# Kernel optimization log

Measured on AMD Instinct MI355X. Metric: run time of the kernel, lower is better.

Reference implementation:

```python
import jax, jax.numpy as jnp
import numpy as np

EPS = 1e-5

def conv1x1(x, w, b):
    # x: (B,C,H,W), w: (O,C), b: (O,)
    return jnp.einsum('bchw,oc->bohw', x, w) + b[None, :, None, None]

def instance_norm(x):
    mu = jnp.mean(x, axis=(2, 3), keepdims=True)
    var = jnp.var(x, axis=(2, 3), keepdims=True)
    return (x - mu) / jnp.sqrt(var + EPS)

def setup_inputs() -> dict:
    key = jax.random.key(0)
    C = 256
    ks = jax.random.split(key, 16)
    def w(k):
        return jax.random.normal(k, (C, C), dtype=jnp.float32) * 0.02
    def b(k):
        return jax.random.normal(k, (C,), dtype=jnp.float32) * 0.01
    return {
        'x': jax.random.normal(ks[0], (8, C, 128, 128), dtype=jnp.float32),
        'wq1': w(ks[1]), 'bq1': b(ks[2]), 'wq2': w(ks[3]), 'bq2': b(ks[4]),
        'wk1': w(ks[5]), 'bk1': b(ks[6]), 'wk2': w(ks[7]), 'bk2': b(ks[8]),
        'wv': w(ks[9]), 'bv': b(ks[10]),
        'wg': w(ks[11]), 'bg': b(ks[12]),
        'wo': w(ks[13]), 'bo': b(ks[14]),
    }

def reference(x, wq1, bq1, wq2, bq2, wk1, bk1, wk2, bk2, wv, bv, wg, bg, wo, bo):
    head = 4
    B, C, H, W = x.shape
    c = C // head  # per-head channels
    n = H * W
    x = instance_norm(x)
    q = jax.nn.softplus(conv1x1(jax.nn.gelu(conv1x1(x, wq1, bq1), approximate=False), wq2, bq2))
    k = jax.nn.softplus(conv1x1(jax.nn.gelu(conv1x1(x, wk1, bk1), approximate=False), wk2, bk2))
    v = jax.nn.gelu(conv1x1(x, wv, bv), approximate=False)
    g = jax.nn.gelu(conv1x1(x, wg, bg), approximate=False)
    # b (head c) h w -> b head c (h w)
    q = q.reshape(B, head, c, n)
    kk = k.reshape(B, head, c, n)
    vv = v.reshape(B, head, c, n)
    kv = jnp.einsum('bhcn,bhdn->bhcd', kk, vv)  # (B,head,c,c)
    scale = 1.0 / jnp.sqrt(jnp.float32(c))
    z = jnp.einsum('bhcn,bhc->bhn', q, kk.sum(axis=-1)) * scale
    z = 1.0 / (z + jnp.float32(n))
    out = jnp.einsum('bhcn,bhcd->bhdn', q, kv) * scale
    out = (out + vv) * z[:, :, None, :]
    out = out.reshape(B, C, H, W)
    out = out * g
    return conv1x1(out, wo, bo)
```

## Files before the change

### kernel.cpp

```cpp
#include <hip/hip_runtime.h>
#include <stdint.h>

typedef short bf8 __attribute__((ext_vector_type(8)));
typedef short s4v __attribute__((ext_vector_type(4)));
typedef float f32x4 __attribute__((ext_vector_type(4)));

__device__ __forceinline__ short f2bf(float f){
  union { float f; unsigned u; } c; c.f = f;
  unsigned r = (c.u + 0x7fffu + ((c.u >> 16) & 1u)) >> 16;
  return (short)r;
}
__device__ __forceinline__ float bf2f(short s){
  union { unsigned u; float f; } c; c.u = ((unsigned)(unsigned short)s) << 16;
  return c.f;
}
__device__ __forceinline__ void gload16(const void* g, void* l){
  __builtin_amdgcn_global_load_lds((const __attribute__((address_space(1))) uint32_t*)g,
                                   (__attribute__((address_space(3))) uint32_t*)l, 16, 0, 0);
}
__device__ __forceinline__ float fast_erf(float x){
  const float s = fabsf(x);
  const float t = __builtin_amdgcn_rcpf(fmaf(0.3275911f, s, 1.0f));
  float p = fmaf(1.061405429f, t, -1.453152027f);
  p = fmaf(p, t, 1.421413741f);
  p = fmaf(p, t, -0.284496736f);
  p = fmaf(p, t, 0.254829592f);
  p = p * t;
  const float e = __expf(-s * s);
  return copysignf(fmaf(-p, e, 1.0f), x);
}
__device__ __forceinline__ float act_gelu(float x){
  return 0.5f * x * (1.0f + fast_erf(x * 0.70710678118654752f));
}
__device__ __forceinline__ float act_softplus(float x){
  const float e = __expf(-fabsf(x));
  return fmaxf(x, 0.0f) + __logf(1.0f + e);
}

__global__ __launch_bounds__(256) void k_stats(const float* __restrict__ x,
                                               float* __restrict__ mu, float* __restrict__ rsig){
  const int row = blockIdx.x;
  const float4* xr = (const float4*)(x + (size_t)row * 16384);
  float s1 = 0.f, s2 = 0.f;
  for (int i = threadIdx.x; i < 4096; i += 256){
    float4 v = xr[i];
    s1 += v.x + v.y + v.z + v.w;
    s2 += v.x*v.x + v.y*v.y + v.z*v.z + v.w*v.w;
  }
  __shared__ float a1[256], a2[256];
  a1[threadIdx.x] = s1; a2[threadIdx.x] = s2; __syncthreads();
  for (int s = 128; s > 0; s >>= 1){
    if (threadIdx.x < s){ a1[threadIdx.x] += a1[threadIdx.x+s]; a2[threadIdx.x] += a2[threadIdx.x+s]; }
    __syncthreads();
  }
  if (threadIdx.x == 0){
    float m = a1[0] * (1.0f/16384.0f);
    float v = a2[0] * (1.0f/16384.0f) - m*m;
    mu[row] = m; rsig[row] = rsqrtf(v + 1e-5f);
  }
}

__global__ __launch_bounds__(256) void k_normt(const float* __restrict__ x, const float* __restrict__ mu,
                                               const float* __restrict__ rsig, short* __restrict__ xn){
  const int n0 = blockIdx.x * 64, c0 = blockIdx.y * 64, b = blockIdx.z;
  __shared__ short lt[64][68];
  const int t = threadIdx.x;
  const int nj = (t & 15) * 4, cb = t >> 4;
#pragma unroll
  for (int it = 0; it < 4; ++it){
    const int ci = cb + it * 16;
    const int row = b * 256 + c0 + ci;
    const float m = mu[row], rs = rsig[row];
    float4 v = *(const float4*)(x + (size_t)row * 16384 + n0 + nj);
    s4v o;
    o[0] = f2bf((v.x - m) * rs); o[1] = f2bf((v.y - m) * rs);
    o[2] = f2bf((v.z - m) * rs); o[3] = f2bf((v.w - m) * rs);
    *(s4v*)(&lt[ci][nj]) = o;
  }
  __syncthreads();
#pragma unroll
  for (int p = 0; p < 2; ++p){
    const int q = p * 256 + t;
    const int nl = q >> 3, c8 = (q & 7) * 8;
    bf8 o;
#pragma unroll
    for (int j = 0; j < 8; ++j) o[j] = lt[c8 + j][nl];
    *(bf8*)(xn + ((size_t)(b * 16384 + n0 + nl)) * 256 + c0 + c8) = o;
  }
}

__global__ __launch_bounds__(256) void k_wconv(const float* w0, const float* w1, const float* w2,
                                               const float* w3, const float* w4, const float* w5,
                                               const float* w6, short* __restrict__ wb){
  const int gid = blockIdx.x * 256 + threadIdx.x;
  const int mat = gid >> 14, r4 = gid & 16383;
  const float* srcs[7] = {w0, w1, w2, w3, w4, w5, w6};
  float4 v = *(const float4*)(srcs[mat] + (size_t)r4 * 4);
  s4v o; o[0] = f2bf(v.x); o[1] = f2bf(v.y); o[2] = f2bf(v.z); o[3] = f2bf(v.w);
  *(s4v*)(wb + (size_t)mat * 65536 + r4 * 4) = o;
}

template<int ACT, int OUTMODE>
__global__ __launch_bounds__(256, 2)
void k_gemm(const short* __restrict__ A, const short* __restrict__ W,
            const float* __restrict__ bias, void* __restrict__ outv){
  __shared__ short sm[12288];
  short* sA = sm;
  short* sB = sm + 4096;
  const int t = threadIdx.x, l = t & 63, w = t >> 6;
  const int wr = w >> 1, wc = w & 1;
  const int lm = l & 15, lk = l >> 4;
  const size_t m0 = (size_t)blockIdx.x * 128;
  const int swz = ((lk ^ ((lm >> 1) & 3)) << 4);
  f32x4 acc[4][8] = {};

  for (int ks = 0; ks < 8; ++ks){
    const int k0 = ks * 32;
#pragma unroll
    for (int p = 0; p < 2; ++p){
      const int q = p * 256 + t, r = q >> 2, kc = q & 3;
      gload16(A + (m0 + r) * 256 + k0 + ((kc ^ ((r >> 1) & 3)) << 3),
              (char*)sA + (p * 256 + w * 64) * 16);
    }
#pragma unroll
    for (int p = 0; p < 4; ++p){
      const int q = p * 256 + t, r = q >> 2, kc = q & 3;
      gload16(W + (size_t)r * 256 + k0 + ((kc ^ ((r >> 1) & 3)) << 3),
              (char*)sB + (p * 256 + w * 64) * 16);
    }
    __syncthreads();
    bf8 af[4], bfv[8];
#pragma unroll
    for (int mi = 0; mi < 4; ++mi)
      af[mi] = *(const bf8*)((const char*)sA + (wr * 64 + mi * 16 + lm) * 64 + swz);
#pragma unroll
    for (int ni = 0; ni < 8; ++ni)
      bfv[ni] = *(const bf8*)((const char*)sB + (wc * 128 + ni * 16 + lm) * 64 + swz);
#pragma unroll
    for (int mi = 0; mi < 4; ++mi)
#pragma unroll
      for (int ni = 0; ni < 8; ++ni){
        if constexpr (OUTMODE == 0)
          acc[mi][ni] = __builtin_amdgcn_mfma_f32_16x16x32_bf16(bfv[ni], af[mi], acc[mi][ni], 0, 0, 0);
        else
          acc[mi][ni] = __builtin_amdgcn_mfma_f32_16x16x32_bf16(af[mi], bfv[ni], acc[mi][ni], 0, 0, 0);
      }
    __syncthreads();
  }

  if constexpr (OUTMODE == 0){
    short* outp = (short*)outv;
#pragma unroll
    for (int ni = 0; ni < 8; ++ni){
      const int ob = wc * 128 + ni * 16 + lk * 4;
      const float4 b4 = *(const float4*)(bias + ob);
#pragma unroll
      for (int mi = 0; mi < 4; ++mi){
        const int px = wr * 64 + mi * 16 + lm;
        s4v o4;
#pragma unroll
        for (int j = 0; j < 4; ++j){
          float v = acc[mi][ni][j] + ((const float*)&b4)[j];
          if (ACT == 1) v = act_gelu(v);
          else if (ACT == 2) v = act_softplus(v);
          o4[j] = f2bf(v);
        }
        *(s4v*)(outp + (m0 + px) * 256 + ob) = o4;
      }
    }
  } else {
    float* outp = (float*)outv;
    const size_t b = m0 >> 14;
    const int nb = (int)(m0 & 16383);
#pragma unroll
    for (int mi = 0; mi < 4; ++mi){
      const int np = nb + wr * 64 + mi * 16 + lk * 4;
#pragma unroll
      for (int ni = 0; ni < 8; ++ni){
        const int o = wc * 128 + ni * 16 + lm;
        const float bi = bias[o];
        float4 v;
        v.x = acc[mi][ni][0] + bi; v.y = acc[mi][ni][1] + bi;
        v.z = acc[mi][ni][2] + bi; v.w = acc[mi][ni][3] + bi;
        *(float4*)(outp + ((b * 256 + o) * 16384 + np)) = v;
      }
    }
  }
}

__global__ __launch_bounds__(256, 2)
void k_chain(const short* __restrict__ A, const short* __restrict__ W1, const float* __restrict__ b1,
             const short* __restrict__ W2, const float* __restrict__ b2, short* __restrict__ out){
  __shared__ short sA[64 * 32];
  __shared__ short sB[256 * 32];
  __shared__ short h1[64 * 256];
  const int t = threadIdx.x, l = t & 63, w = t >> 6;
  const int lm = l & 15, lk = l >> 4;
  const size_t m0 = (size_t)blockIdx.x * 64;
  const int swz = ((lk ^ ((lm >> 1) & 3)) << 4);
  f32x4 acc[4][4] = {};

  for (int ks = 0; ks < 8; ++ks){
    const int k0 = ks * 32;
    {
      const int r = t >> 2, kc = t & 3;
      gload16(A + (m0 + r) * 256 + k0 + ((kc ^ ((r >> 1) & 3)) << 3),
              (char*)sA + w * 1024);
    }
#pragma unroll
    for (int p = 0; p < 4; ++p){
      const int q = p * 256 + t, r = q >> 2, kc = q & 3;
      gload16(W1 + (size_t)r * 256 + k0 + ((kc ^ ((r >> 1) & 3)) << 3),
              (char*)sB + (p * 256 + w * 64) * 16);
    }
    __syncthreads();
    bf8 af[4], bfv[4];
#pragma unroll
    for (int mi = 0; mi < 4; ++mi)
      af[mi] = *(const bf8*)((const char*)sA + (mi * 16 + lm) * 64 + swz);
#pragma unroll
    for (int ni = 0; ni < 4; ++ni)
      bfv[ni] = *(const bf8*)((const char*)sB + (w * 64 + ni * 16 + lm) * 64 + swz);
#pragma unroll
    for (int mi = 0; mi < 4; ++mi)
#pragma unroll
      for (int ni = 0; ni < 4; ++ni)
        acc[mi][ni] = __builtin_amdgcn_mfma_f32_16x16x32_bf16(bfv[ni], af[mi], acc[mi][ni], 0, 0, 0);
    __syncthreads();
  }
#pragma unroll
  for (int ni = 0; ni < 4; ++ni){
    const int ob = w * 64 + ni * 16 + lk * 4;
    const float4 b4 = *(const float4*)(b1 + ob);
#pragma unroll
    for (int mi = 0; mi < 4; ++mi){
      const int px = mi * 16 + lm;
      s4v o4;
#pragma unroll
      for (int j = 0; j < 4; ++j)
        o4[j] = f2bf(act_gelu(acc[mi][ni][j] + ((const float*)&b4)[j]));
      const int slot = (ob >> 3) ^ (px & 7);
      *(s4v*)((char*)h1 + px * 512 + (slot << 4) + (ob & 4) * 2) = o4;
      acc[mi][ni] = (f32x4){0.f, 0.f, 0.f, 0.f};
    }
  }
  __syncthreads();

  for (int ks = 0; ks < 8; ++ks){
    const int k0 = ks * 32;
#pragma unroll
    for (int p = 0; p < 4; ++p){
      const int q = p * 256 + t, r = q >> 2, kc = q & 3;
      gload16(W2 + (size_t)r * 256 + k0 + ((kc ^ ((r >> 1) & 3)) << 3),
              (char*)sB + (p * 256 + w * 64) * 16);
    }
    __syncthreads();
    bf8 af[4], bfv[4];
#pragma unroll
    for (int mi = 0; mi < 4; ++mi){
      const int row = mi * 16 + lm;
      const int slot = (ks * 4 + lk) ^ (row & 7);
      af[mi] = *(const bf8*)((const char*)h1 + row * 512 + (slot << 4));
    }
#pragma unroll
    for (int ni = 0; ni < 4; ++ni)
      bfv[ni] = *(const bf8*)((const char*)sB + (w * 64 + ni * 16 + lm) * 64 + swz);
#pragma unroll
    for (int mi = 0; mi < 4; ++mi)
#pragma unroll
      for (int ni = 0; ni < 4; ++ni)
        acc[mi][ni] = __builtin_amdgcn_mfma_f32_16x16x32_bf16(bfv[ni], af[mi], acc[mi][ni], 0, 0, 0);
    __syncthreads();
  }
#pragma unroll
  for (int ni = 0; ni < 4; ++ni){
    const int ob = w * 64 + ni * 16 + lk * 4;
    const float4 b4 = *(const float4*)(b2 + ob);
#pragma unroll
    for (int mi = 0; mi < 4; ++mi){
      const int px = mi * 16 + lm;
      s4v o4;
#pragma unroll
      for (int j = 0; j < 4; ++j)
        o4[j] = f2bf(act_softplus(acc[mi][ni][j] + ((const float*)&b4)[j]));
      *(s4v*)(out + (m0 + px) * 256 + ob) = o4;
    }
  }
}

__global__ __launch_bounds__(256) void k_kv(const short* __restrict__ kg, const short* __restrict__ vg,
                                            float* __restrict__ kvpart, float* __restrict__ kspart){
  const int s = blockIdx.x, h = blockIdx.y, b = blockIdx.z;
  __shared__ short sk[64 * 72], sv[64 * 72];
  __shared__ float pl[256][8];
  const int t = threadIdx.x, l = t & 63, w = t >> 6;
  const int lm = l & 15, lk = l >> 4;
  float ksp[8];
#pragma unroll
  for (int j = 0; j < 8; ++j) ksp[j] = 0.f;
  f32x4 acc[4] = {};
  const size_t rowbase = ((size_t)b * 16384 + s * 2048) * 256 + h * 64;

  for (int tt = 0; tt < 32; ++tt){
    __syncthreads();
#pragma unroll
    for (int p = 0; p < 2; ++p){
      const int q = p * 256 + t;
      const int nl = q >> 3, c8 = (q & 7) * 8;
      bf8 kvv = *(const bf8*)(kg + rowbase + (size_t)(tt * 64 + nl) * 256 + c8);
      bf8 vvv = *(const bf8*)(vg + rowbase + (size_t)(tt * 64 + nl) * 256 + c8);
#pragma unroll
      for (int j = 0; j < 8; ++j){
        sk[(c8 + j) * 72 + nl] = kvv[j];
        sv[(c8 + j) * 72 + nl] = vvv[j];
        ksp[j] += bf2f(kvv[j]);
      }
    }
    __syncthreads();
#pragma unroll
    for (int ks = 0; ks < 2; ++ks){
      bf8 ak = *(const bf8*)((const char*)sk + (w * 16 + lm) * 144 + ks * 64 + lk * 16);
#pragma unroll
      for (int ni = 0; ni < 4; ++ni){
        bf8 bv = *(const bf8*)((const char*)sv + (ni * 16 + lm) * 144 + ks * 64 + lk * 16);
        acc[ni] = __builtin_amdgcn_mfma_f32_16x16x32_bf16(ak, bv, acc[ni], 0, 0, 0);
      }
    }
  }
#pragma unroll
  for (int j = 0; j < 8; ++j) pl[t][j] = ksp[j];
  __syncthreads();
  const size_t slot = (size_t)(b * 4 + h) * 8 + s;
  if (t < 64){
    float sum = 0.f;
    const int g8 = t >> 3, j = t & 7;
    for (int m = 0; m < 32; ++m) sum += pl[m * 8 + g8][j];
    kspart[slot * 64 + t] = sum;
  }
  float* kvp = kvpart + slot * 4096;
#pragma unroll
  for (int ni = 0; ni < 4; ++ni)
#pragma unroll
    for (int j = 0; j < 4; ++j){
      const int c = w * 16 + lk * 4 + j, d = ni * 16 + lm;
      kvp[c * 64 + d] = acc[ni][j];
    }
}

__global__ __launch_bounds__(256) void k_kvred(const float* __restrict__ kvpart, const float* __restrict__ kspart,
                                               short* __restrict__ kvT, float* __restrict__ ksum_s){
  const int gid = blockIdx.x * 256 + threadIdx.x;
#pragma unroll
  for (int i = 0; i < 8; ++i){
    const int o = gid * 8 + i;
    const int bh = o >> 12, rem = o & 4095, d = rem >> 6, c = rem & 63;
    float sum = 0.f;
#pragma unroll
    for (int s = 0; s < 8; ++s) sum += kvpart[((size_t)bh * 8 + s) * 4096 + c * 64 + d];
    kvT[o] = f2bf(sum * 0.125f);
  }
  if (gid < 2048){
    float sum = 0.f;
#pragma unroll
    for (int s = 0; s < 8; ++s) sum += kspart[((size_t)(gid >> 6) * 8 + s) * 64 + (gid & 63)];
    ksum_s[gid] = sum * 0.125f;
  }
}

__global__ __launch_bounds__(256, 3) void k_attn(const short* __restrict__ qg, const short* __restrict__ vg,
                                                 const short* __restrict__ gg, const short* __restrict__ kvT,
                                                 const float* __restrict__ ksum_s, short* __restrict__ y){
  const int n0 = blockIdx.x * 64, b = blockIdx.y;
  __shared__ short skv[256 * 72];
  __shared__ float sz[256];
  __shared__ float sks[256];
  const int t = threadIdx.x, l = t & 63, w = t >> 6;
  const int lm = l & 15, lk = l >> 4;
  const size_t mrow = (size_t)b * 16384 + n0;
  const int h = w;

  const short* kvb = kvT + (size_t)b * 16384;
#pragma unroll
  for (int it = 0; it < 8; ++it){
    const int q = it * 256 + t, r = q >> 3, c8 = (q & 7) * 8;
    *(bf8*)((char*)skv + r * 144 + c8 * 2) = *(const bf8*)(kvb + r * 64 + c8);
  }
  sks[t] = ksum_s[b * 256 + t];
  __syncthreads();

  {
    const int p = l;
    float dot = 0.f;
#pragma unroll
    for (int cc = 0; cc < 8; ++cc){
      bf8 qv = *(const bf8*)(qg + (mrow + p) * 256 + h * 64 + cc * 8);
#pragma unroll
      for (int j = 0; j < 8; ++j) dot += bf2f(qv[j]) * sks[h * 64 + cc * 8 + j];
    }
    sz[h * 64 + p] = 1.0f / (dot + 16384.0f);
  }

  f32x4 acc[4][4] = {};
#pragma unroll
  for (int ks = 0; ks < 2; ++ks){
    bf8 aq[4];
#pragma unroll
    for (int mi = 0; mi < 4; ++mi)
      aq[mi] = *(const bf8*)(qg + (mrow + mi * 16 + lm) * 256 + h * 64 + ks * 32 + lk * 8);
#pragma unroll
    for (int ni = 0; ni < 4; ++ni){
      bf8 bk = *(const bf8*)((const char*)skv + (h * 64 + ni * 16 + lm) * 144 + ks * 64 + lk * 16);
#pragma unroll
      for (int mi = 0; mi < 4; ++mi)
        acc[mi][ni] = __builtin_amdgcn_mfma_f32_16x16x32_bf16(bk, aq[mi], acc[mi][ni], 0, 0, 0);
    }
  }
#pragma unroll
  for (int mi = 0; mi < 4; ++mi){
    const int px = mi * 16 + lm;
    const float zf = sz[h * 64 + px];
    const size_t base = (mrow + px) * 256;
#pragma unroll
    for (int ni = 0; ni < 4; ++ni){
      const int ch = h * 64 + ni * 16 + lk * 4;
      s4v v4 = *(const s4v*)(vg + base + ch);
      s4v g4 = *(const s4v*)(gg + base + ch);
      s4v o4;
#pragma unroll
      for (int j = 0; j < 4; ++j)
        o4[j] = f2bf((acc[mi][ni][j] + bf2f(v4[j])) * zf * bf2f(g4[j]));
      *(s4v*)(y + base + ch) = o4;
    }
  }
}

extern "C" void kernel_launch(void* const* d_in, const int* in_sizes, int n_in,
                              void* d_out, int out_size, void* d_ws, size_t ws_size,
                              hipStream_t stream){
  (void)in_sizes; (void)n_in; (void)out_size; (void)ws_size;
  const float* x   = (const float*)d_in[0];
  const float* wq1 = (const float*)d_in[1];
  const float* bq1 = (const float*)d_in[2];
  const float* wq2 = (const float*)d_in[3];
  const float* bq2 = (const float*)d_in[4];
  const float* wk1 = (const float*)d_in[5];
  const float* bk1 = (const float*)d_in[6];
  const float* wk2 = (const float*)d_in[7];
  const float* bk2 = (const float*)d_in[8];
  const float* wv  = (const float*)d_in[9];
  const float* bv  = (const float*)d_in[10];
  const float* wg  = (const float*)d_in[11];
  const float* bg  = (const float*)d_in[12];
  const float* wo  = (const float*)d_in[13];
  const float* bo  = (const float*)d_in[14];

  char* ws = (char*)d_ws;
  float* mu     = (float*)(ws + 0);
  float* rsig   = (float*)(ws + 8192);
  short* wb     = (short*)(ws + 16384);
  float* kvpart = (float*)(ws + 933888);
  float* kspart = (float*)(ws + 5128192);
  short* kvT    = (short*)(ws + 5193728);
  float* ksum_s = (float*)(ws + 5455872);
  short* B0 = (short*)(ws + 8388608);
  short* B1 = B0 + 33554432;
  short* B2 = B1 + 33554432;
  short* B3 = B2 + 33554432;

  k_wconv<<<448, 256, 0, stream>>>(wq1, wq2, wk1, wk2, wv, wg, wo, wb);
  k_stats<<<2048, 256, 0, stream>>>(x, mu, rsig);
  k_normt<<<dim3(256, 4, 8), 256, 0, stream>>>(x, mu, rsig, B0);
  k_chain<<<2048, 256, 0, stream>>>(B0, wb + 0 * 65536, bq1, wb + 1 * 65536, bq2, B2);
  k_chain<<<2048, 256, 0, stream>>>(B0, wb + 2 * 65536, bk1, wb + 3 * 65536, bk2, B3);
  k_gemm<1, 0><<<1024, 256, 0, stream>>>(B0, wb + 4 * 65536, bv, B1);
  k_kv<<<dim3(8, 4, 8), 256, 0, stream>>>(B3, B1, kvpart, kspart);
  k_kvred<<<64, 256, 0, stream>>>(kvpart, kspart, kvT, ksum_s);
  k_gemm<1, 0><<<1024, 256, 0, stream>>>(B0, wb + 5 * 65536, bg, B3);
  k_attn<<<dim3(256, 8), 256, 0, stream>>>(B2, B1, B3, kvT, ksum_s, B0);
  k_gemm<0, 1><<<1024, 256, 0, stream>>>(B0, wb + 6 * 65536, bo, d_out);
}
```

Measured before the change: 494.4 us.

## Fuse stats into transpose pass and load GEMM operands directly from global

Instance-norm statistics are now computed as per-block partial sums inside the transpose pass. The raw bf16 transpose is then normalized in place by a separate elementwise kernel after a small reduction kernel, so the fp32 input is read only once instead of twice. The GEMM, chain and attention kernels drop LDS staging and barriers and load MFMA operands straight from global memory, relying on cache reuse. k_attn occupancy is also raised. The risks are extra bf16 rounding before normalization, an added read-write pass over the activation buffer, and uncoalesced, uncached-reuse global loads in the GEMMs.

```diff
diff --git a/kernel.cpp b/kernel.cpp
--- a/kernel.cpp
+++ b/kernel.cpp
@@ -13,10 +13,6 @@
 __device__ __forceinline__ float bf2f(short s){
   union { unsigned u; float f; } c; c.u = ((unsigned)(unsigned short)s) << 16;
   return c.f;
-}
-__device__ __forceinline__ void gload16(const void* g, void* l){
-  __builtin_amdgcn_global_load_lds((const __attribute__((address_space(1))) uint32_t*)g,
-                                   (__attribute__((address_space(3))) uint32_t*)l, 16, 0, 0);
 }
 __device__ __forceinline__ float fast_erf(float x){
   const float s = fabsf(x);
@@ -37,45 +33,22 @@
   return fmaxf(x, 0.0f) + __logf(1.0f + e);
 }
 
-__global__ __launch_bounds__(256) void k_stats(const float* __restrict__ x,
-                                               float* __restrict__ mu, float* __restrict__ rsig){
-  const int row = blockIdx.x;
-  const float4* xr = (const float4*)(x + (size_t)row * 16384);
-  float s1 = 0.f, s2 = 0.f;
-  for (int i = threadIdx.x; i < 4096; i += 256){
-    float4 v = xr[i];
-    s1 += v.x + v.y + v.z + v.w;
-    s2 += v.x*v.x + v.y*v.y + v.z*v.z + v.w*v.w;
-  }
-  __shared__ float a1[256], a2[256];
-  a1[threadIdx.x] = s1; a2[threadIdx.x] = s2; __syncthreads();
-  for (int s = 128; s > 0; s >>= 1){
-    if (threadIdx.x < s){ a1[threadIdx.x] += a1[threadIdx.x+s]; a2[threadIdx.x] += a2[threadIdx.x+s]; }
-    __syncthreads();
-  }
-  if (threadIdx.x == 0){
-    float m = a1[0] * (1.0f/16384.0f);
-    float v = a2[0] * (1.0f/16384.0f) - m*m;
-    mu[row] = m; rsig[row] = rsqrtf(v + 1e-5f);
-  }
-}
-
-__global__ __launch_bounds__(256) void k_normt(const float* __restrict__ x, const float* __restrict__ mu,
-                                               const float* __restrict__ rsig, short* __restrict__ xn){
+__global__ __launch_bounds__(256) void k_statst(const float* __restrict__ x, short* __restrict__ xt,
+                                                float* __restrict__ ps1, float* __restrict__ ps2){
   const int n0 = blockIdx.x * 64, c0 = blockIdx.y * 64, b = blockIdx.z;
   __shared__ short lt[64][68];
-  const int t = threadIdx.x;
-  const int nj = (t & 15) * 4, cb = t >> 4;
+  const int t = threadIdx.x, nj = (t & 15) * 4, cb = t >> 4;
+  float s1[4] = {0.f,0.f,0.f,0.f}, s2[4] = {0.f,0.f,0.f,0.f};
 #pragma unroll
   for (int it = 0; it < 4; ++it){
     const int ci = cb + it * 16;
     const int row = b * 256 + c0 + ci;
-    const float m = mu[row], rs = rsig[row];
     float4 v = *(const float4*)(x + (size_t)row * 16384 + n0 + nj);
     s4v o;
-    o[0] = f2bf((v.x - m) * rs); o[1] = f2bf((v.y - m) * rs);
-    o[2] = f2bf((v.z - m) * rs); o[3] = f2bf((v.w - m) * rs);
+    o[0] = f2bf(v.x); o[1] = f2bf(v.y); o[2] = f2bf(v.z); o[3] = f2bf(v.w);
     *(s4v*)(&lt[ci][nj]) = o;
+    s1[it] += v.x + v.y + v.z + v.w;
+    s2[it] += v.x*v.x + v.y*v.y + v.z*v.z + v.w*v.w;
   }
   __syncthreads();
 #pragma unroll
@@ -85,7 +58,64 @@
     bf8 o;
 #pragma unroll
     for (int j = 0; j < 8; ++j) o[j] = lt[c8 + j][nl];
-    *(bf8*)(xn + ((size_t)(b * 16384 + n0 + nl)) * 256 + c0 + c8) = o;
+    *(bf8*)(xt + ((size_t)(b * 16384 + n0 + nl)) * 256 + c0 + c8) = o;
+  }
+#pragma unroll
+  for (int it = 0; it < 4; ++it){
+#pragma unroll
+    for (int off = 8; off > 0; off >>= 1){
+      s1[it] += __shfl_down(s1[it], off);
+      s2[it] += __shfl_down(s2[it], off);
+    }
+  }
+  if ((t & 15) == 0){
+#pragma unroll
+    for (int it = 0; it < 4; ++it){
+      const int c = c0 + cb + it * 16;
+      ps1[((size_t)(b * 256 + c)) * 256 + blockIdx.x] = s1[it];
+      ps2[((size_t)(b * 256 + c)) * 256 + blockIdx.x] = s2[it];
+    }
+  }
+}
+
+__global__ __launch_bounds__(256) void k_red(const float* __restrict__ ps1, const float* __restrict__ ps2,
+                                             float* __restrict__ mu, float* __restrict__ rsig){
+  const int bc = blockIdx.x;
+  const int t = threadIdx.x;
+  __shared__ float a1[256], a2[256];
+  a1[t] = ps1[(size_t)bc * 256 + t];
+  a2[t] = ps2[(size_t)bc * 256 + t];
+  __syncthreads();
+  for (int s = 128; s > 0; s >>= 1){
+    if (t < s){ a1[t] += a1[t+s]; a2[t] += a2[t+s]; }
+    __syncthreads();
+  }
+  if (t == 0){
+    float m = a1[0] * (1.0f/16384.0f);
+    float v = a2[0] * (1.0f/16384.0f) - m*m;
+    mu[bc] = m; rsig[bc] = rsqrtf(v + 1e-5f);
+  }
+}
+
+__global__ __launch_bounds__(256) void k_norm(short* xn, const float* __restrict__ mu,
+                                              const float* __restrict__ rsig){
+  const int g = blockIdx.x * 256 + threadIdx.x;
+#pragma unroll
+  for (int pass = 0; pass < 8; ++pass){
+    const int idx = g + pass * 524288;
+    const int bn = idx >> 5, c8 = idx & 31;
+    const int b = bn >> 14;
+    const float* mp = mu + b * 256 + c8 * 8;
+    const float* rp = rsig + b * 256 + c8 * 8;
+    float4 m0 = *(const float4*)mp, m1 = *(const float4*)(mp + 4);
+    float4 r0 = *(const float4*)rp, r1 = *(const float4*)(rp + 4);
+    float mm[8] = {m0.x,m0.y,m0.z,m0.w,m1.x,m1.y,m1.z,m1.w};
+    float rr[8] = {r0.x,r0.y,r0.z,r0.w,r1.x,r1.y,r1.z,r1.w};
+    bf8 v = *(const bf8*)(xn + (size_t)idx * 8);
+    bf8 o;
+#pragma unroll
+    for (int j = 0; j < 8; ++j) o[j] = f2bf((bf2f(v[j]) - mm[j]) * rr[j]);
+    *(bf8*)(xn + (size_t)idx * 8) = o;
   }
 }
 
@@ -104,38 +134,23 @@
 __global__ __launch_bounds__(256, 2)
 void k_gemm(const short* __restrict__ A, const short* __restrict__ W,
             const float* __restrict__ bias, void* __restrict__ outv){
-  __shared__ short sm[12288];
-  short* sA = sm;
-  short* sB = sm + 4096;
   const int t = threadIdx.x, l = t & 63, w = t >> 6;
   const int wr = w >> 1, wc = w & 1;
   const int lm = l & 15, lk = l >> 4;
   const size_t m0 = (size_t)blockIdx.x * 128;
-  const int swz = ((lk ^ ((lm >> 1) & 3)) << 4);
+  const short* Ab = A + (m0 + wr * 64 + lm) * 256 + lk * 8;
+  const short* Wb = W + (size_t)(wc * 128 + lm) * 256 + lk * 8;
   f32x4 acc[4][8] = {};
 
+#pragma unroll 2
   for (int ks = 0; ks < 8; ++ks){
-    const int k0 = ks * 32;
-#pragma unroll
-    for (int p = 0; p < 2; ++p){
-      const int q = p * 256 + t, r = q >> 2, kc = q & 3;
-      gload16(A + (m0 + r) * 256 + k0 + ((kc ^ ((r >> 1) & 3)) << 3),
-              (char*)sA + (p * 256 + w * 64) * 16);
-    }
-#pragma unroll
-    for (int p = 0; p < 4; ++p){
-      const int q = p * 256 + t, r = q >> 2, kc = q & 3;
-      gload16(W + (size_t)r * 256 + k0 + ((kc ^ ((r >> 1) & 3)) << 3),
-              (char*)sB + (p * 256 + w * 64) * 16);
-    }
-    __syncthreads();
     bf8 af[4], bfv[8];
 #pragma unroll
     for (int mi = 0; mi < 4; ++mi)
-      af[mi] = *(const bf8*)((const char*)sA + (wr * 64 + mi * 16 + lm) * 64 + swz);
+      af[mi] = *(const bf8*)(Ab + mi * 16 * 256 + ks * 32);
 #pragma unroll
     for (int ni = 0; ni < 8; ++ni)
-      bfv[ni] = *(const bf8*)((const char*)sB + (wc * 128 + ni * 16 + lm) * 64 + swz);
+      bfv[ni] = *(const bf8*)(Wb + ni * 16 * 256 + ks * 32);
 #pragma unroll
     for (int mi = 0; mi < 4; ++mi)
 #pragma unroll
@@ -145,7 +160,6 @@
         else
           acc[mi][ni] = __builtin_amdgcn_mfma_f32_16x16x32_bf16(af[mi], bfv[ni], acc[mi][ni], 0, 0, 0);
       }
-    __syncthreads();
   }
 
   if constexpr (OUTMODE == 0){
@@ -191,42 +205,29 @@
 __global__ __launch_bounds__(256, 2)
 void k_chain(const short* __restrict__ A, const short* __restrict__ W1, const float* __restrict__ b1,
              const short* __restrict__ W2, const float* __restrict__ b2, short* __restrict__ out){
-  __shared__ short sA[64 * 32];
-  __shared__ short sB[256 * 32];
   __shared__ short h1[64 * 256];
   const int t = threadIdx.x, l = t & 63, w = t >> 6;
   const int lm = l & 15, lk = l >> 4;
   const size_t m0 = (size_t)blockIdx.x * 64;
-  const int swz = ((lk ^ ((lm >> 1) & 3)) << 4);
+  const short* Ab = A + (m0 + lm) * 256 + lk * 8;
+  const short* W1b = W1 + (size_t)(w * 64 + lm) * 256 + lk * 8;
+  const short* W2b = W2 + (size_t)(w * 64 + lm) * 256 + lk * 8;
   f32x4 acc[4][4] = {};
 
+#pragma unroll 2
   for (int ks = 0; ks < 8; ++ks){
-    const int k0 = ks * 32;
-    {
-      const int r = t >> 2, kc = t & 3;
-      gload16(A + (m0 + r) * 256 + k0 + ((kc ^ ((r >> 1) & 3)) << 3),
-              (char*)sA + w * 1024);
-    }
-#pragma unroll
-    for (int p = 0; p < 4; ++p){
-      const int q = p * 256 + t, r = q >> 2, kc = q & 3;
-      gload16(W1 + (size_t)r * 256 + k0 + ((kc ^ ((r >> 1) & 3)) << 3),
-              (char*)sB + (p * 256 + w * 64) * 16);
-    }
-    __syncthreads();
     bf8 af[4], bfv[4];
 #pragma unroll
     for (int mi = 0; mi < 4; ++mi)
-      af[mi] = *(const bf8*)((const char*)sA + (mi * 16 + lm) * 64 + swz);
+      af[mi] = *(const bf8*)(Ab + mi * 16 * 256 + ks * 32);
 #pragma unroll
     for (int ni = 0; ni < 4; ++ni)
-      bfv[ni] = *(const bf8*)((const char*)sB + (w * 64 + ni * 16 + lm) * 64 + swz);
+      bfv[ni] = *(const bf8*)(W1b + ni * 16 * 256 + ks * 32);
 #pragma unroll
     for (int mi = 0; mi < 4; ++mi)
 #pragma unroll
       for (int ni = 0; ni < 4; ++ni)
         acc[mi][ni] = __builtin_amdgcn_mfma_f32_16x16x32_bf16(bfv[ni], af[mi], acc[mi][ni], 0, 0, 0);
-    __syncthreads();
   }
 #pragma unroll
   for (int ni = 0; ni < 4; ++ni){
@@ -246,15 +247,8 @@
   }
   __syncthreads();
 
+#pragma unroll 2
   for (int ks = 0; ks < 8; ++ks){
-    const int k0 = ks * 32;
-#pragma unroll
-    for (int p = 0; p < 4; ++p){
-      const int q = p * 256 + t, r = q >> 2, kc = q & 3;
-      gload16(W2 + (size_t)r * 256 + k0 + ((kc ^ ((r >> 1) & 3)) << 3),
-              (char*)sB + (p * 256 + w * 64) * 16);
-    }
-    __syncthreads();
     bf8 af[4], bfv[4];
 #pragma unroll
     for (int mi = 0; mi < 4; ++mi){
@@ -264,13 +258,12 @@
     }
 #pragma unroll
     for (int ni = 0; ni < 4; ++ni)
-      bfv[ni] = *(const bf8*)((const char*)sB + (w * 64 + ni * 16 + lm) * 64 + swz);
+      bfv[ni] = *(const bf8*)(W2b + ni * 16 * 256 + ks * 32);
 #pragma unroll
     for (int mi = 0; mi < 4; ++mi)
 #pragma unroll
       for (int ni = 0; ni < 4; ++ni)
         acc[mi][ni] = __builtin_amdgcn_mfma_f32_16x16x32_bf16(bfv[ni], af[mi], acc[mi][ni], 0, 0, 0);
-    __syncthreads();
   }
 #pragma unroll
   for (int ni = 0; ni < 4; ++ni){
@@ -367,11 +360,10 @@
   }
 }
 
-__global__ __launch_bounds__(256, 3) void k_attn(const short* __restrict__ qg, const short* __restrict__ vg,
+__global__ __launch_bounds__(256, 4) void k_attn(const short* __restrict__ qg, const short* __restrict__ vg,
                                                  const short* __restrict__ gg, const short* __restrict__ kvT,
                                                  const float* __restrict__ ksum_s, short* __restrict__ y){
   const int n0 = blockIdx.x * 64, b = blockIdx.y;
-  __shared__ short skv[256 * 72];
   __shared__ float sz[256];
   __shared__ float sks[256];
   const int t = threadIdx.x, l = t & 63, w = t >> 6;
@@ -379,14 +371,7 @@
   const size_t mrow = (size_t)b * 16384 + n0;
   const int h = w;
 
-  const short* kvb = kvT + (size_t)b * 16384;
-#pragma unroll
-  for (int it = 0; it < 8; ++it){
-    const int q = it * 256 + t, r = q >> 3, c8 = (q & 7) * 8;
-    *(bf8*)((char*)skv + r * 144 + c8 * 2) = *(const bf8*)(kvb + r * 64 + c8);
-  }
   sks[t] = ksum_s[b * 256 + t];
-  __syncthreads();
 
   {
     const int p = l;
@@ -400,6 +385,7 @@
     sz[h * 64 + p] = 1.0f / (dot + 16384.0f);
   }
 
+  const short* kvb = kvT + (size_t)b * 16384;
   f32x4 acc[4][4] = {};
 #pragma unroll
   for (int ks = 0; ks < 2; ++ks){
@@ -409,7 +395,7 @@
       aq[mi] = *(const bf8*)(qg + (mrow + mi * 16 + lm) * 256 + h * 64 + ks * 32 + lk * 8);
 #pragma unroll
     for (int ni = 0; ni < 4; ++ni){
-      bf8 bk = *(const bf8*)((const char*)skv + (h * 64 + ni * 16 + lm) * 144 + ks * 64 + lk * 16);
+      bf8 bk = *(const bf8*)(kvb + (size_t)(h * 64 + ni * 16 + lm) * 64 + ks * 32 + lk * 8);
 #pragma unroll
       for (int mi = 0; mi < 4; ++mi)
         acc[mi][ni] = __builtin_amdgcn_mfma_f32_16x16x32_bf16(bk, aq[mi], acc[mi][ni], 0, 0, 0);
@@ -459,6 +445,8 @@
   float* rsig   = (float*)(ws + 8192);
   short* wb     = (short*)(ws + 16384);
   float* kvpart = (float*)(ws + 933888);
+  float* ps1    = (float*)(ws + 933888);
+  float* ps2    = (float*)(ws + 3031040);
   float* kspart = (float*)(ws + 5128192);
   short* kvT    = (short*)(ws + 5193728);
   float* ksum_s = (float*)(ws + 5455872);
@@ -468,8 +456,9 @@
   short* B3 = B2 + 33554432;
 
   k_wconv<<<448, 256, 0, stream>>>(wq1, wq2, wk1, wk2, wv, wg, wo, wb);
-  k_stats<<<2048, 256, 0, stream>>>(x, mu, rsig);
-  k_normt<<<dim3(256, 4, 8), 256, 0, stream>>>(x, mu, rsig, B0);
+  k_statst<<<dim3(256, 4, 8), 256, 0, stream>>>(x, B0, ps1, ps2);
+  k_red<<<2048, 256, 0, stream>>>(ps1, ps2, mu, rsig);
+  k_norm<<<2048, 256, 0, stream>>>(B0, mu, rsig);
   k_chain<<<2048, 256, 0, stream>>>(B0, wb + 0 * 65536, bq1, wb + 1 * 65536, bq2, B2);
   k_chain<<<2048, 256, 0, stream>>>(B0, wb + 2 * 65536, bk1, wb + 3 * 65536, bk2, B3);
   k_gemm<1, 0><<<1024, 256, 0, stream>>>(B0, wb + 4 * 65536, bv, B1);
```

New measurement: 619.4 us. 25.3% more time.
